# Optimization experiments

Hardware: AMD Instinct MI355X
Metric: run time of the kernel (lower is better)

The kernel has to match this reference:

```python
import jax, jax.numpy as jnp
import numpy as np

D_MODEL = 1024
NUM_EXP = 64
EPS = 1e-9
B, L = 16, 2048


def setup_inputs() -> dict:
    key = jax.random.key(0)
    ks = jax.random.split(key, 12)
    s = 1.0 / np.sqrt(D_MODEL)
    inp = {
        "x": jax.random.normal(ks[0], (B, L, D_MODEL), dtype=jnp.float32),
        "n_indexes": jax.random.randint(ks[1], (B, NUM_EXP), 0, NUM_EXP),
        "mask": jax.random.randint(ks[2], (B, 1, L), 0, 2).astype(jnp.int32),
        "q_emb": jax.random.normal(ks[3], (NUM_EXP, D_MODEL), dtype=jnp.float32),
        "b_emb": jax.random.normal(ks[4], (NUM_EXP, D_MODEL), dtype=jnp.float32),
        "Wk": jax.random.normal(ks[5], (D_MODEL, D_MODEL), dtype=jnp.float32) * s,
        "bk": jnp.zeros((D_MODEL,), jnp.float32),
        "Wa": jax.random.normal(ks[6], (D_MODEL, D_MODEL), dtype=jnp.float32) * s,
        "ba": jnp.zeros((D_MODEL,), jnp.float32),
        "Wb": jax.random.normal(ks[7], (D_MODEL, D_MODEL), dtype=jnp.float32) * s,
        "bb": jnp.zeros((D_MODEL,), jnp.float32),
        "Ws": jax.random.normal(ks[8], (D_MODEL, D_MODEL), dtype=jnp.float32) * s,
        "bs": jnp.zeros((D_MODEL,), jnp.float32),
    }
    return inp


def reference(x, n_indexes, mask, q_emb, b_emb, Wk, bk, Wa, ba, Wb, bb, Ws, bs):
    # Dropout layers act as identity (eval mode).
    query_exp = q_emb[n_indexes]          # [B, E, D]
    bias_exp = b_emb[n_indexes]           # [B, E, D]
    x_key = x @ Wk.T + bk                 # [B, L, D]
    z = jnp.einsum('bed,bld->bel', query_exp, x_key) / np.sqrt(D_MODEL)  # [B, E, L]

    maskf = (mask != 0).astype(z.dtype)   # broadcast [B,1,L]
    class_a_fw = jax.nn.relu(z) * maskf
    class_b_fw = jax.nn.relu(-z) * maskf
    class_a_fw = class_a_fw / (class_a_fw.sum(-1, keepdims=True) + EPS)
    class_b_fw = class_b_fw / (class_b_fw.sum(-1, keepdims=True) + EPS)

    class_a = jnp.einsum('bel,bld->bed', class_a_fw, x @ Wa.T + ba) + bias_exp
    class_b = jnp.einsum('bel,bld->bed', class_b_fw, x @ Wb.T + bb) + bias_exp

    zt = jnp.swapaxes(z, -2, -1)          # [B, L, E]  (unmasked, as in source)
    class_a_bw = jax.nn.relu(zt)
    class_b_bw = jax.nn.relu(-zt)
    class_a_bw = class_a_bw / (class_a_bw.sum(-1, keepdims=True) + EPS)
    class_b_bw = class_b_bw / (class_b_bw.sum(-1, keepdims=True) + EPS)

    class_a = jnp.einsum('ble,bed->bld', class_a_bw, class_a)  # [B, L, D]
    class_b = jnp.einsum('ble,bed->bld', class_b_bw, class_b)

    selector = jax.nn.sigmoid(x @ Ws.T + bs)
    return selector * class_a + (1.0 - selector) * class_b
```

## Files before the change

### kernel.cpp

```cpp
#include <hip/hip_runtime.h>
#include <math.h>

#define D_MODEL 1024
#define NUM_EXP 64
#define B_SZ 16
#define L_SZ 2048

using bf16x8  = __attribute__((ext_vector_type(8))) __bf16;
using floatx4 = __attribute__((ext_vector_type(4))) float;
using ushort8 = __attribute__((ext_vector_type(8))) unsigned short;
using ushort4v = __attribute__((ext_vector_type(4))) unsigned short;

__device__ __forceinline__ unsigned short f2bf(float f) {
    union { float f; unsigned u; } x; x.f = f;
    unsigned r = (x.u + 0x7fffu + ((x.u >> 16) & 1u)) >> 16;
    return (unsigned short)r;
}
__device__ __forceinline__ float bf2f(unsigned short h) {
    union { unsigned u; float f; } x; x.u = ((unsigned)h) << 16;
    return x.f;
}

#define GLD16(gp, lp) __builtin_amdgcn_global_load_lds( \
    (const __attribute__((address_space(1))) unsigned int*)(gp), \
    (__attribute__((address_space(3))) unsigned int*)(lp), 16, 0, 0)

__global__ void k_convx(const float* __restrict__ in, unsigned short* __restrict__ outN,
                        unsigned short* __restrict__ outT)
{
    __shared__ unsigned short T[64][65];
    const int b = blockIdx.z;
    const int l0 = blockIdx.y * 64, c0 = blockIdx.x * 64;
    const int t = threadIdx.x;
    const int tr = t >> 4, tc = (t & 15) * 4;
    const float* src = in + ((long)b * L_SZ + l0) * D_MODEL + c0;
    unsigned short* dN = outN + ((long)b * L_SZ + l0) * D_MODEL + c0;
    #pragma unroll
    for (int i = 0; i < 4; i++) {
        int r = tr + i * 16;
        float4 v = *(const float4*)(src + (long)r * D_MODEL + tc);
        ushort4v u; u[0]=f2bf(v.x); u[1]=f2bf(v.y); u[2]=f2bf(v.z); u[3]=f2bf(v.w);
        *(ushort4v*)(dN + (long)r * D_MODEL + tc) = u;
        T[r][tc+0]=u[0]; T[r][tc+1]=u[1]; T[r][tc+2]=u[2]; T[r][tc+3]=u[3];
    }
    __syncthreads();
    unsigned short* dT = outT + ((long)b * D_MODEL + c0) * L_SZ + l0;
    #pragma unroll
    for (int i = 0; i < 4; i++) {
        int c = tr + i * 16;
        ushort4v u;
        u[0]=T[tc+0][c]; u[1]=T[tc+1][c]; u[2]=T[tc+2][c]; u[3]=T[tc+3][c];
        *(ushort4v*)(dT + (long)c * L_SZ + tc) = u;
    }
}

__global__ void k_transw(const float* __restrict__ in, unsigned short* __restrict__ outT)
{
    __shared__ unsigned short T[64][65];
    const int r0 = blockIdx.y * 64, c0 = blockIdx.x * 64;
    const int t = threadIdx.x;
    const int tr = t >> 4, tc = (t & 15) * 4;
    const float* src = in + (long)r0 * D_MODEL + c0;
    #pragma unroll
    for (int i = 0; i < 4; i++) {
        int r = tr + i * 16;
        float4 v = *(const float4*)(src + (long)r * D_MODEL + tc);
        T[r][tc+0]=f2bf(v.x); T[r][tc+1]=f2bf(v.y); T[r][tc+2]=f2bf(v.z); T[r][tc+3]=f2bf(v.w);
    }
    __syncthreads();
    unsigned short* dT = outT + ((long)c0) * D_MODEL + r0;
    #pragma unroll
    for (int i = 0; i < 4; i++) {
        int c = tr + i * 16;
        ushort4v u;
        u[0]=T[tc+0][c]; u[1]=T[tc+1][c]; u[2]=T[tc+2][c]; u[3]=T[tc+3][c];
        *(ushort4v*)(dT + (long)c * D_MODEL + tc) = u;
    }
}

__global__ void k_convert3(const float* __restrict__ a, const float* __restrict__ b,
                           const float* __restrict__ c,
                           unsigned short* __restrict__ oa, unsigned short* __restrict__ ob,
                           unsigned short* __restrict__ oc)
{
    long i = ((long)blockIdx.x * 256 + threadIdx.x) * 8;
    int which = (int)(i >> 20);
    long off = i & ((1L << 20) - 1);
    const float* src = which == 0 ? a : which == 1 ? b : c;
    unsigned short* dst = which == 0 ? oa : which == 1 ? ob : oc;
    float4 v0 = *(const float4*)(src + off);
    float4 v1 = *(const float4*)(src + off + 4);
    ushort8 r;
    r[0]=f2bf(v0.x); r[1]=f2bf(v0.y); r[2]=f2bf(v0.z); r[3]=f2bf(v0.w);
    r[4]=f2bf(v1.x); r[5]=f2bf(v1.y); r[6]=f2bf(v1.z); r[7]=f2bf(v1.w);
    *(ushort8*)(dst + off) = r;
}

__global__ void k_gather(const int* __restrict__ idx, const float* __restrict__ q_emb,
                         const float* __restrict__ b_emb, const float* __restrict__ bk,
                         unsigned short* __restrict__ qexp, float* __restrict__ bias_exp,
                         float* __restrict__ qbk)
{
    int be = blockIdx.x;
    int row = idx[be];
    int t = threadIdx.x;
    const float* qs = q_emb + (long)row * D_MODEL;
    const float* bsrc = b_emb + (long)row * D_MODEL;
    float4 q4 = *(const float4*)(qs + t * 4);
    float4 k4 = *(const float4*)(bk + t * 4);
    float4 b4 = *(const float4*)(bsrc + t * 4);
    ushort4v r; r[0]=f2bf(q4.x); r[1]=f2bf(q4.y); r[2]=f2bf(q4.z); r[3]=f2bf(q4.w);
    *(ushort4v*)(qexp + (long)be * D_MODEL + t * 4) = r;
    *(float4*)(bias_exp + (long)be * D_MODEL + t * 4) = b4;
    float p = q4.x*k4.x + q4.y*k4.y + q4.z*k4.z + q4.w*k4.w;
    #pragma unroll
    for (int o = 32; o > 0; o >>= 1) p += __shfl_down(p, o);
    __shared__ float red[4];
    if ((t & 63) == 0) red[t >> 6] = p;
    __syncthreads();
    if (t == 0) qbk[be] = red[0] + red[1] + red[2] + red[3];
}

__launch_bounds__(256)
__global__ void k_gemm_bt(const unsigned short* __restrict__ A,
                          const unsigned short* __restrict__ Bm,
                          const float* __restrict__ rowbias,
                          void* __restrict__ Cout,
                          int M, int N, int K, float scale, int flags,
                          long sA, long sB, long sC)
{
    __shared__ __align__(16) unsigned short As[64 * 32];
    __shared__ __align__(16) unsigned short Bs[64 * 32];
    const int bz = blockIdx.z;
    const unsigned short* Ab = A + (long)bz * sA;
    const unsigned short* Bb = Bm + (long)bz * sB;
    const int tid = threadIdx.x;
    const int wave = tid >> 6, lane = tid & 63;
    const int m0 = blockIdx.y * 64, n0 = blockIdx.x * 64;
    const int lrow = tid >> 2, lk = (tid & 3) * 8;
    const int q = lane >> 4, mr = lane & 15;

    floatx4 acc[4];
    floatx4 z4 = {0.f, 0.f, 0.f, 0.f};
    #pragma unroll
    for (int j = 0; j < 4; j++) acc[j] = z4;

    const unsigned short* Aptr = Ab + (long)(m0 + lrow) * K + lk;
    const unsigned short* Bptr = Bb + (long)(n0 + lrow) * K + lk;

    for (int k0 = 0; k0 < K; k0 += 32) {
        __syncthreads();
        *(ushort8*)&As[lrow * 32 + lk] = *(const ushort8*)(Aptr + k0);
        *(ushort8*)&Bs[lrow * 32 + lk] = *(const ushort8*)(Bptr + k0);
        __syncthreads();
        bf16x8 af = *(const bf16x8*)&As[(wave * 16 + mr) * 32 + q * 8];
        #pragma unroll
        for (int j = 0; j < 4; j++) {
            bf16x8 bfr = *(const bf16x8*)&Bs[(j * 16 + mr) * 32 + q * 8];
            acc[j] = __builtin_amdgcn_mfma_f32_16x16x32_bf16(af, bfr, acc[j], 0, 0, 0);
        }
    }
    #pragma unroll
    for (int j = 0; j < 4; j++) {
        int gn = n0 + j * 16 + mr;
        #pragma unroll
        for (int r = 0; r < 4; r++) {
            int gm = m0 + wave * 16 + q * 4 + r;
            float v = acc[j][r];
            if (rowbias) v += rowbias[(long)bz * M + gm];
            v *= scale;
            long cidx = (long)bz * sC + (long)gm * N + gn;
            if (flags & 1) ((unsigned short*)Cout)[cidx] = f2bf(v);
            else           ((float*)Cout)[cidx] = v;
        }
    }
}

__launch_bounds__(256)
__global__ void k_gemm_fw2(const unsigned short* __restrict__ A1,
                           const unsigned short* __restrict__ A2,
                           const unsigned short* __restrict__ Bt,
                           unsigned short* __restrict__ C1,
                           unsigned short* __restrict__ C2)
{
    __shared__ __align__(16) unsigned short As1[64 * 32];
    __shared__ __align__(16) unsigned short As2[64 * 32];
    __shared__ __align__(16) unsigned short Bs[64 * 32];
    const int bz = blockIdx.z;
    const int n0 = blockIdx.x * 64;
    const int tid = threadIdx.x;
    const int wave = tid >> 6, lane = tid & 63;
    const int lrow = tid >> 2, lk = (tid & 3) * 8;
    const int q = lane >> 4, mr = lane & 15;

    const unsigned short* a1p = A1 + ((long)bz * NUM_EXP + lrow) * L_SZ + lk;
    const unsigned short* a2p = A2 + ((long)bz * NUM_EXP + lrow) * L_SZ + lk;
    const unsigned short* bp  = Bt + ((long)bz * D_MODEL + n0 + lrow) * L_SZ + lk;

    floatx4 acc1[4], acc2[4];
    floatx4 z4 = {0.f, 0.f, 0.f, 0.f};
    #pragma unroll
    for (int j = 0; j < 4; j++) { acc1[j] = z4; acc2[j] = z4; }

    for (int k0 = 0; k0 < L_SZ; k0 += 32) {
        __syncthreads();
        *(ushort8*)&As1[lrow * 32 + lk] = *(const ushort8*)(a1p + k0);
        *(ushort8*)&As2[lrow * 32 + lk] = *(const ushort8*)(a2p + k0);
        *(ushort8*)&Bs[lrow * 32 + lk]  = *(const ushort8*)(bp + k0);
        __syncthreads();
        bf16x8 f1 = *(const bf16x8*)&As1[(wave * 16 + mr) * 32 + q * 8];
        bf16x8 f2 = *(const bf16x8*)&As2[(wave * 16 + mr) * 32 + q * 8];
        #pragma unroll
        for (int j = 0; j < 4; j++) {
            bf16x8 bb = *(const bf16x8*)&Bs[(j * 16 + mr) * 32 + q * 8];
            acc1[j] = __builtin_amdgcn_mfma_f32_16x16x32_bf16(f1, bb, acc1[j], 0, 0, 0);
            acc2[j] = __builtin_amdgcn_mfma_f32_16x16x32_bf16(f2, bb, acc2[j], 0, 0, 0);
        }
    }
    #pragma unroll
    for (int j = 0; j < 4; j++) {
        int gn = n0 + j * 16 + mr;
        #pragma unroll
        for (int r = 0; r < 4; r++) {
            int gm = wave * 16 + q * 4 + r;
            long cidx = ((long)bz * NUM_EXP + gm) * D_MODEL + gn;
            C1[cidx] = f2bf(acc1[j][r]);
            C2[cidx] = f2bf(acc2[j][r]);
        }
    }
}

__launch_bounds__(256)
__global__ void k_gemm_cls(const unsigned short* __restrict__ fwxA, const unsigned short* __restrict__ fwxB,
                           const unsigned short* __restrict__ Wa_, const unsigned short* __restrict__ Wb_,
                           const float* __restrict__ ba_, const float* __restrict__ bb_,
                           const float* __restrict__ wsA, const float* __restrict__ wsB,
                           const float* __restrict__ biasE,
                           unsigned short* __restrict__ aHi, unsigned short* __restrict__ aLo,
                           unsigned short* __restrict__ bHi, unsigned short* __restrict__ bLo)
{
    __shared__ __align__(16) unsigned short As[64 * 32];
    __shared__ __align__(16) unsigned short Bs[64 * 32];
    const int zz = blockIdx.z;
    const int side = zz >> 4, bz = zz & 15;
    const unsigned short* Ab = (side ? fwxB : fwxA) + (long)bz * NUM_EXP * D_MODEL;
    const unsigned short* Bb = side ? Wb_ : Wa_;
    const float* cb = side ? bb_ : ba_;
    const float* rw = (side ? wsB : wsA) + bz * NUM_EXP;
    const float* bE = biasE + (long)bz * NUM_EXP * D_MODEL;
    unsigned short* oHi = (side ? bHi : aHi) + (long)bz * NUM_EXP * D_MODEL;
    unsigned short* oLo = (side ? bLo : aLo) + (long)bz * NUM_EXP * D_MODEL;

    const int tid = threadIdx.x;
    const int wave = tid >> 6, lane = tid & 63;
    const int n0 = blockIdx.x * 64;
    const int lrow = tid >> 2, lk = (tid & 3) * 8;
    const int q = lane >> 4, mr = lane & 15;

    floatx4 acc[4];
    floatx4 z4 = {0.f, 0.f, 0.f, 0.f};
    #pragma unroll
    for (int j = 0; j < 4; j++) acc[j] = z4;

    const unsigned short* Aptr = Ab + (long)lrow * D_MODEL + lk;
    const unsigned short* Bptr = Bb + (long)(n0 + lrow) * D_MODEL + lk;

    for (int k0 = 0; k0 < D_MODEL; k0 += 32) {
        __syncthreads();
        *(ushort8*)&As[lrow * 32 + lk] = *(const ushort8*)(Aptr + k0);
        *(ushort8*)&Bs[lrow * 32 + lk] = *(const ushort8*)(Bptr + k0);
        __syncthreads();
        bf16x8 af = *(const bf16x8*)&As[(wave * 16 + mr) * 32 + q * 8];
        #pragma unroll
        for (int j = 0; j < 4; j++) {
            bf16x8 bfr = *(const bf16x8*)&Bs[(j * 16 + mr) * 32 + q * 8];
            acc[j] = __builtin_amdgcn_mfma_f32_16x16x32_bf16(af, bfr, acc[j], 0, 0, 0);
        }
    }
    #pragma unroll
    for (int j = 0; j < 4; j++) {
        int gn = n0 + j * 16 + mr;
        float cbv = cb[gn];
        #pragma unroll
        for (int r = 0; r < 4; r++) {
            int gm = wave * 16 + q * 4 + r;
            float v = acc[j][r] + rw[gm] * cbv + bE[(long)gm * D_MODEL + gn];
            unsigned short hi = f2bf(v);
            long tix = (long)gn * NUM_EXP + gm;
            oHi[tix] = hi;
            oLo[tix] = f2bf(v - bf2f(hi));
        }
    }
}

__launch_bounds__(512, 2)
__global__ void k_gemm_sel(const unsigned short* __restrict__ A,
                           const unsigned short* __restrict__ Bm,
                           const float* __restrict__ bias,
                           unsigned short* __restrict__ C)
{
    __shared__ __align__(16) unsigned short As[2][2][8192];
    __shared__ __align__(16) unsigned short Bs[2][2][8192];

    const int tid = threadIdx.x;
    const int wid = tid >> 6, lane = tid & 63;
    const int q = lane >> 4, mr = lane & 15;
    const int wm = wid >> 2, wn = wid & 3;
    const int kread = (q ^ ((mr >> 1) & 3)) * 8;

    const int bid = blockIdx.x;
    const int wg = (bid & 7) * 64 + (bid >> 3);
    const int m0 = (wg >> 2) * 256;
    const int n0 = (wg & 3) * 256;

    const unsigned short* Ag = A + (long)m0 * 1024;
    const unsigned short* Bg = Bm + (long)n0 * 1024;

    const int srow = tid >> 2;
    const int sgrp = (tid & 3) ^ ((srow >> 1) & 3);
    const long soff = (long)srow * 1024 + sgrp * 8;
    const int ldst = wid * 64 * 8;

    auto STAGE = [&](int g) {
        int tile = g >> 2; if (tile > 15) tile = 15;
        const int kh = (g >> 1) & 1, isB = g & 1;
        const unsigned short* src = (isB ? Bg : Ag) + (long)tile * 64 + kh * 32 + soff;
        unsigned short* dst = (isB ? &Bs[0][0][0] : &As[0][0][0])
                              + ((tile & 1) * 2 + kh) * 8192 + ldst;
        GLD16(src, dst);
        GLD16(src + 128 * 1024, dst + 4096);
    };

    floatx4 acc[8][4];
    floatx4 z4 = {0.f, 0.f, 0.f, 0.f};
    #pragma unroll
    for (int i = 0; i < 8; i++)
        #pragma unroll
        for (int j = 0; j < 4; j++) acc[i][j] = z4;

    STAGE(0); STAGE(1); STAGE(2); STAGE(3); STAGE(4); STAGE(5);
    asm volatile("s_waitcnt vmcnt(4)" ::: "memory");
    __builtin_amdgcn_s_barrier();

    for (int t = 0; t < 16; t++) {
        const unsigned short* Abuf = &As[t & 1][0][0];
        const unsigned short* Bbuf = &Bs[t & 1][0][0];
        bf16x8 bfr[4];
        #pragma unroll
        for (int p = 0; p < 4; p++) {
            const int kh = p >> 1, mh = p & 1;
            bf16x8 af[4];
            #pragma unroll
            for (int i = 0; i < 4; i++)
                af[i] = *(const bf16x8*)&Abuf[kh * 8192 +
                        (wm * 128 + mh * 64 + i * 16 + mr) * 32 + kread];
            if (mh == 0) {
                #pragma unroll
                for (int j = 0; j < 4; j++)
                    bfr[j] = *(const bf16x8*)&Bbuf[kh * 8192 +
                             (wn * 64 + j * 16 + mr) * 32 + kread];
            }
            STAGE(4 * t + p + 6);
            if (mh == 1) asm volatile("s_waitcnt vmcnt(8)" ::: "memory");
            __builtin_amdgcn_s_barrier();
            asm volatile("s_waitcnt lgkmcnt(0)" ::: "memory");
            __builtin_amdgcn_sched_barrier(0);
            __builtin_amdgcn_s_setprio(1);
            #pragma unroll
            for (int i = 0; i < 4; i++)
                #pragma unroll
                for (int j = 0; j < 4; j++)
                    acc[mh * 4 + i][j] = __builtin_amdgcn_mfma_f32_16x16x32_bf16(
                        af[i], bfr[j], acc[mh * 4 + i][j], 0, 0, 0);
            __builtin_amdgcn_s_setprio(0);
            __builtin_amdgcn_s_barrier();
            __builtin_amdgcn_sched_barrier(0);
        }
    }
    asm volatile("s_waitcnt vmcnt(0)" ::: "memory");

    #pragma unroll
    for (int i = 0; i < 8; i++) {
        #pragma unroll
        for (int j = 0; j < 4; j++) {
            const int gn = n0 + wn * 64 + j * 16 + mr;
            const float cbv = bias[gn];
            #pragma unroll
            for (int r = 0; r < 4; r++) {
                const int gm = m0 + wm * 128 + i * 16 + q * 4 + r;
                C[(long)gm * 1024 + gn] = f2bf(acc[i][j][r] + cbv);
            }
        }
    }
}

__global__ void k_fwnorm(const float* __restrict__ z, const int* __restrict__ mask,
                         unsigned short* __restrict__ a_fw, unsigned short* __restrict__ b_fw,
                         float* __restrict__ wsum_a, float* __restrict__ wsum_b)
{
    int be = blockIdx.x;
    int b = be >> 6;
    const float* zr = z + (long)be * L_SZ;
    const int* mr = mask + (long)b * L_SZ;
    int tid = threadIdx.x;
    float sa = 0.f, sb = 0.f;
    for (int l = tid; l < L_SZ; l += 256) {
        float v = zr[l];
        if (mr[l] != 0) { sa += fmaxf(v, 0.f); sb += fmaxf(-v, 0.f); }
    }
    #pragma unroll
    for (int o = 32; o > 0; o >>= 1) { sa += __shfl_down(sa, o); sb += __shfl_down(sb, o); }
    __shared__ float red[8];
    int wave = tid >> 6, lane = tid & 63;
    if (lane == 0) { red[wave] = sa; red[4 + wave] = sb; }
    __syncthreads();
    float ta = red[0] + red[1] + red[2] + red[3];
    float tb = red[4] + red[5] + red[6] + red[7];
    float ia = 1.f / (ta + 1e-9f), ib = 1.f / (tb + 1e-9f);
    if (tid == 0) { wsum_a[be] = ta * ia; wsum_b[be] = tb * ib; }
    for (int l = tid; l < L_SZ; l += 256) {
        float v = zr[l];
        float m = (mr[l] != 0) ? 1.f : 0.f;
        a_fw[(long)be * L_SZ + l] = f2bf(fmaxf(v, 0.f) * m * ia);
        b_fw[(long)be * L_SZ + l] = f2bf(fmaxf(-v, 0.f) * m * ib);
    }
}

__global__ void k_bwnorm(const float* __restrict__ z, unsigned short* __restrict__ a_bw,
                         unsigned short* __restrict__ b_bw)
{
    int r = blockIdx.x * 256 + threadIdx.x;
    int b = r >> 11, l = r & 2047;
    const float* zb = z + (long)b * NUM_EXP * L_SZ + l;
    float sa = 0.f, sb = 0.f;
    float va[NUM_EXP];
    #pragma unroll 8
    for (int e = 0; e < NUM_EXP; e++) {
        float v = zb[(long)e * L_SZ];
        va[e] = v;
        sa += fmaxf(v, 0.f); sb += fmaxf(-v, 0.f);
    }
    float ia = 1.f / (sa + 1e-9f), ib = 1.f / (sb + 1e-9f);
    unsigned short* ar = a_bw + (long)r * NUM_EXP;
    unsigned short* br = b_bw + (long)r * NUM_EXP;
    #pragma unroll 8
    for (int e = 0; e < NUM_EXP; e++) {
        float v = va[e];
        ar[e] = f2bf(fmaxf(v, 0.f) * ia);
        br[e] = f2bf(fmaxf(-v, 0.f) * ib);
    }
}

__launch_bounds__(256)
__global__ void k_final_mfma(const unsigned short* __restrict__ aw,
                             const unsigned short* __restrict__ bw,
                             const unsigned short* __restrict__ caHi,
                             const unsigned short* __restrict__ caLo,
                             const unsigned short* __restrict__ cbHi,
                             const unsigned short* __restrict__ cbLo,
                             const unsigned short* __restrict__ selbf,
                             float* __restrict__ out)
{
    __shared__ __align__(16) unsigned short Aa[64 * 72];
    __shared__ __align__(16) unsigned short Ab[64 * 72];
    __shared__ __align__(16) unsigned short BaH[64 * 72];
    __shared__ __align__(16) unsigned short BaL[64 * 72];
    __shared__ __align__(16) unsigned short BbH[64 * 72];
    __shared__ __align__(16) unsigned short BbL[64 * 72];
    const int bz = blockIdx.z;
    const int l0 = blockIdx.y * 64, d0 = blockIdx.x * 64;
    const int tid = threadIdx.x;
    const int wave = tid >> 6, lane = tid & 63;
    const int q = lane >> 4, mr = lane & 15;

    const unsigned short* awb = aw + ((long)bz * L_SZ + l0) * NUM_EXP;
    const unsigned short* bwb = bw + ((long)bz * L_SZ + l0) * NUM_EXP;
    const long cbase = ((long)bz * D_MODEL + d0) * NUM_EXP;

    #pragma unroll
    for (int c = 0; c < 2; c++) {
        int idx = c * 256 + tid;
        int row = idx >> 3, kc = (idx & 7) * 8;
        int lw = row * 72 + kc;
        long ga = (long)row * NUM_EXP + kc;
        *(ushort8*)&Aa[lw]  = *(const ushort8*)(awb + ga);
        *(ushort8*)&Ab[lw]  = *(const ushort8*)(bwb + ga);
        *(ushort8*)&BaH[lw] = *(const ushort8*)(caHi + cbase + ga);
        *(ushort8*)&BaL[lw] = *(const ushort8*)(caLo + cbase + ga);
        *(ushort8*)&BbH[lw] = *(const ushort8*)(cbHi + cbase + ga);
        *(ushort8*)&BbL[lw] = *(const ushort8*)(cbLo + cbase + ga);
    }
    __syncthreads();

    floatx4 accA[4], accB[4];
    floatx4 z4 = {0.f, 0.f, 0.f, 0.f};
    #pragma unroll
    for (int j = 0; j < 4; j++) { accA[j] = z4; accB[j] = z4; }

    #pragma unroll
    for (int ks = 0; ks < 2; ks++) {
        int ko = ks * 32 + q * 8;
        bf16x8 fa = *(const bf16x8*)&Aa[(wave * 16 + mr) * 72 + ko];
        bf16x8 fb = *(const bf16x8*)&Ab[(wave * 16 + mr) * 72 + ko];
        #pragma unroll
        for (int j = 0; j < 4; j++) {
            int bo = (j * 16 + mr) * 72 + ko;
            accA[j] = __builtin_amdgcn_mfma_f32_16x16x32_bf16(fa, *(const bf16x8*)&BaH[bo], accA[j], 0, 0, 0);
            accA[j] = __builtin_amdgcn_mfma_f32_16x16x32_bf16(fa, *(const bf16x8*)&BaL[bo], accA[j], 0, 0, 0);
            accB[j] = __builtin_amdgcn_mfma_f32_16x16x32_bf16(fb, *(const bf16x8*)&BbH[bo], accB[j], 0, 0, 0);
            accB[j] = __builtin_amdgcn_mfma_f32_16x16x32_bf16(fb, *(const bf16x8*)&BbL[bo], accB[j], 0, 0, 0);
        }
    }

    #pragma unroll
    for (int j = 0; j < 4; j++) {
        #pragma unroll
        for (int r = 0; r < 4; r++) {
            int gl = l0 + wave * 16 + q * 4 + r;
            int gd = d0 + j * 16 + mr;
            long o = ((long)bz * L_SZ + gl) * D_MODEL + gd;
            float s = 1.f / (1.f + __expf(-bf2f(selbf[o])));
            out[o] = s * accA[j][r] + (1.f - s) * accB[j][r];
        }
    }
}

extern "C" void kernel_launch(void* const* d_in, const int* in_sizes, int n_in,
                              void* d_out, int out_size, void* d_ws, size_t ws_size,
                              hipStream_t stream)
{
    const float* x     = (const float*)d_in[0];
    const int*   nidx  = (const int*)d_in[1];
    const int*   mask  = (const int*)d_in[2];
    const float* q_emb = (const float*)d_in[3];
    const float* b_emb = (const float*)d_in[4];
    const float* Wk    = (const float*)d_in[5];
    const float* bk    = (const float*)d_in[6];
    const float* Wa    = (const float*)d_in[7];
    const float* ba    = (const float*)d_in[8];
    const float* Wb    = (const float*)d_in[9];
    const float* bb    = (const float*)d_in[10];
    const float* Ws    = (const float*)d_in[11];
    const float* bs    = (const float*)d_in[12];
    float* out = (float*)d_out;

    constexpr long BLD = (long)B_SZ * L_SZ * D_MODEL;
    constexpr long BEL = (long)B_SZ * NUM_EXP * L_SZ;
    constexpr long BED = (long)B_SZ * NUM_EXP * D_MODEL;
    constexpr long DD  = (long)D_MODEL * D_MODEL;

    char* w = (char*)d_ws;
    size_t off = 0;
    auto carve = [&](size_t bytes) { char* p = w + off; off += (bytes + 255) & ~(size_t)255; return p; };
    unsigned short* x_bf   = (unsigned short*)carve(BLD * 2);
    unsigned short* x_bfT  = (unsigned short*)carve(BLD * 2);
    unsigned short* wkT_bf = (unsigned short*)carve(DD * 2);
    unsigned short* wa_bf  = (unsigned short*)carve(DD * 2);
    unsigned short* wb_bf  = (unsigned short*)carve(DD * 2);
    unsigned short* ws_bf  = (unsigned short*)carve(DD * 2);
    unsigned short* qexp   = (unsigned short*)carve(BED * 2);
    float*          bias_e = (float*)carve(BED * 4);
    float*          qbk    = (float*)carve(B_SZ * NUM_EXP * 4);
    unsigned short* qk     = (unsigned short*)carve(BED * 2);
    float*          z      = (float*)carve(BEL * 4);
    unsigned short* a_fw   = (unsigned short*)carve(BEL * 2);
    unsigned short* b_fw   = (unsigned short*)carve(BEL * 2);
    float*          wsum_a = (float*)carve(B_SZ * NUM_EXP * 4);
    float*          wsum_b = (float*)carve(B_SZ * NUM_EXP * 4);
    unsigned short* a_bw   = (unsigned short*)carve(BEL * 2);
    unsigned short* b_bw   = (unsigned short*)carve(BEL * 2);
    unsigned short* fwx_a  = (unsigned short*)carve(BED * 2);
    unsigned short* fwx_b  = (unsigned short*)carve(BED * 2);
    unsigned short* caHi   = (unsigned short*)carve(BED * 2);
    unsigned short* caLo   = (unsigned short*)carve(BED * 2);
    unsigned short* cbHi   = (unsigned short*)carve(BED * 2);
    unsigned short* cbLo   = (unsigned short*)carve(BED * 2);
    if (ws_size < off) return;
    unsigned short* selbf = x_bfT;

    k_convx<<<dim3(16, 32, B_SZ), 256, 0, stream>>>(x, x_bf, x_bfT);
    k_transw<<<dim3(16, 16), 256, 0, stream>>>(Wk, wkT_bf);
    k_convert3<<<(3 * DD) / 2048, 256, 0, stream>>>(Wa, Wb, Ws, wa_bf, wb_bf, ws_bf);
    k_gather<<<B_SZ * NUM_EXP, 256, 0, stream>>>(nidx, q_emb, b_emb, bk, qexp, bias_e, qbk);

    k_gemm_bt<<<dim3(16, 1, B_SZ), 256, 0, stream>>>(qexp, wkT_bf, nullptr, qk,
        NUM_EXP, D_MODEL, D_MODEL, 1.f, 1, (long)NUM_EXP * D_MODEL, 0, (long)NUM_EXP * D_MODEL);

    k_gemm_bt<<<dim3(32, 1, B_SZ), 256, 0, stream>>>(qk, x_bf, qbk, z,
        NUM_EXP, L_SZ, D_MODEL, 1.f / 32.f, 0,
        (long)NUM_EXP * D_MODEL, (long)L_SZ * D_MODEL, (long)NUM_EXP * L_SZ);

    k_fwnorm<<<B_SZ * NUM_EXP, 256, 0, stream>>>(z, mask, a_fw, b_fw, wsum_a, wsum_b);
    k_bwnorm<<<(B_SZ * L_SZ) / 256, 256, 0, stream>>>(z, a_bw, b_bw);

    k_gemm_fw2<<<dim3(16, 1, B_SZ), 256, 0, stream>>>(a_fw, b_fw, x_bfT, fwx_a, fwx_b);

    k_gemm_sel<<<512, 512, 0, stream>>>(x_bf, ws_bf, bs, selbf);

    k_gemm_cls<<<dim3(16, 1, 32), 256, 0, stream>>>(fwx_a, fwx_b, wa_bf, wb_bf, ba, bb,
        wsum_a, wsum_b, bias_e, caHi, caLo, cbHi, cbLo);

    k_final_mfma<<<dim3(16, 32, B_SZ), 256, 0, stream>>>(a_bw, b_bw, caHi, caLo, cbHi, cbLo, selbf, out);
}
```

Measured before the change: 548.4 us.

## Merge prep and norm kernels, split-K fw2 GEMM, halve sel GEMM grid

Combines the Wk transpose, the weight conversion and the gather into one k_prep launch, and combines the forward and backward normalisations into one k_norms launch, which removes launch overhead. k_gemm_fw2 becomes a 512-thread block that splits the L reduction between two groups and adds the partials through shared memory. With only 256 blocks, this targets the low occupancy of that GEMM. k_gemm_sel now has each workgroup compute two adjacent 256-wide N tiles in sequence, halving its grid, at the cost of fewer parallel blocks and a longer serial loop.

```diff
diff --git a/kernel.cpp b/kernel.cpp
--- a/kernel.cpp
+++ b/kernel.cpp
@@ -54,71 +54,70 @@
     }
 }
 
-__global__ void k_transw(const float* __restrict__ in, unsigned short* __restrict__ outT)
+__global__ void k_prep(const float* __restrict__ Wk,
+                       const float* __restrict__ Wa, const float* __restrict__ Wb,
+                       const float* __restrict__ Ws,
+                       const int* __restrict__ idx, const float* __restrict__ q_emb,
+                       const float* __restrict__ b_emb, const float* __restrict__ bk,
+                       unsigned short* __restrict__ wkT,
+                       unsigned short* __restrict__ oa, unsigned short* __restrict__ ob,
+                       unsigned short* __restrict__ oc,
+                       unsigned short* __restrict__ qexp, float* __restrict__ bias_exp,
+                       float* __restrict__ qbk)
 {
     __shared__ unsigned short T[64][65];
-    const int r0 = blockIdx.y * 64, c0 = blockIdx.x * 64;
+    __shared__ float red[4];
+    const int blk = blockIdx.x;
     const int t = threadIdx.x;
-    const int tr = t >> 4, tc = (t & 15) * 4;
-    const float* src = in + (long)r0 * D_MODEL + c0;
-    #pragma unroll
-    for (int i = 0; i < 4; i++) {
-        int r = tr + i * 16;
-        float4 v = *(const float4*)(src + (long)r * D_MODEL + tc);
-        T[r][tc+0]=f2bf(v.x); T[r][tc+1]=f2bf(v.y); T[r][tc+2]=f2bf(v.z); T[r][tc+3]=f2bf(v.w);
-    }
-    __syncthreads();
-    unsigned short* dT = outT + ((long)c0) * D_MODEL + r0;
-    #pragma unroll
-    for (int i = 0; i < 4; i++) {
-        int c = tr + i * 16;
-        ushort4v u;
-        u[0]=T[tc+0][c]; u[1]=T[tc+1][c]; u[2]=T[tc+2][c]; u[3]=T[tc+3][c];
-        *(ushort4v*)(dT + (long)c * D_MODEL + tc) = u;
-    }
-}
-
-__global__ void k_convert3(const float* __restrict__ a, const float* __restrict__ b,
-                           const float* __restrict__ c,
-                           unsigned short* __restrict__ oa, unsigned short* __restrict__ ob,
-                           unsigned short* __restrict__ oc)
-{
-    long i = ((long)blockIdx.x * 256 + threadIdx.x) * 8;
-    int which = (int)(i >> 20);
-    long off = i & ((1L << 20) - 1);
-    const float* src = which == 0 ? a : which == 1 ? b : c;
-    unsigned short* dst = which == 0 ? oa : which == 1 ? ob : oc;
-    float4 v0 = *(const float4*)(src + off);
-    float4 v1 = *(const float4*)(src + off + 4);
-    ushort8 r;
-    r[0]=f2bf(v0.x); r[1]=f2bf(v0.y); r[2]=f2bf(v0.z); r[3]=f2bf(v0.w);
-    r[4]=f2bf(v1.x); r[5]=f2bf(v1.y); r[6]=f2bf(v1.z); r[7]=f2bf(v1.w);
-    *(ushort8*)(dst + off) = r;
-}
-
-__global__ void k_gather(const int* __restrict__ idx, const float* __restrict__ q_emb,
-                         const float* __restrict__ b_emb, const float* __restrict__ bk,
-                         unsigned short* __restrict__ qexp, float* __restrict__ bias_exp,
-                         float* __restrict__ qbk)
-{
-    int be = blockIdx.x;
-    int row = idx[be];
-    int t = threadIdx.x;
-    const float* qs = q_emb + (long)row * D_MODEL;
-    const float* bsrc = b_emb + (long)row * D_MODEL;
-    float4 q4 = *(const float4*)(qs + t * 4);
-    float4 k4 = *(const float4*)(bk + t * 4);
-    float4 b4 = *(const float4*)(bsrc + t * 4);
-    ushort4v r; r[0]=f2bf(q4.x); r[1]=f2bf(q4.y); r[2]=f2bf(q4.z); r[3]=f2bf(q4.w);
-    *(ushort4v*)(qexp + (long)be * D_MODEL + t * 4) = r;
-    *(float4*)(bias_exp + (long)be * D_MODEL + t * 4) = b4;
-    float p = q4.x*k4.x + q4.y*k4.y + q4.z*k4.z + q4.w*k4.w;
-    #pragma unroll
-    for (int o = 32; o > 0; o >>= 1) p += __shfl_down(p, o);
-    __shared__ float red[4];
-    if ((t & 63) == 0) red[t >> 6] = p;
-    __syncthreads();
-    if (t == 0) qbk[be] = red[0] + red[1] + red[2] + red[3];
+    if (blk < 256) {
+        const int r0 = (blk >> 4) * 64, c0 = (blk & 15) * 64;
+        const int tr = t >> 4, tc = (t & 15) * 4;
+        const float* src = Wk + (long)r0 * D_MODEL + c0;
+        #pragma unroll
+        for (int i = 0; i < 4; i++) {
+            int r = tr + i * 16;
+            float4 v = *(const float4*)(src + (long)r * D_MODEL + tc);
+            T[r][tc+0]=f2bf(v.x); T[r][tc+1]=f2bf(v.y); T[r][tc+2]=f2bf(v.z); T[r][tc+3]=f2bf(v.w);
+        }
+        __syncthreads();
+        unsigned short* dT = wkT + ((long)c0) * D_MODEL + r0;
+        #pragma unroll
+        for (int i = 0; i < 4; i++) {
+            int c = tr + i * 16;
+            ushort4v u;
+            u[0]=T[tc+0][c]; u[1]=T[tc+1][c]; u[2]=T[tc+2][c]; u[3]=T[tc+3][c];
+            *(ushort4v*)(dT + (long)c * D_MODEL + tc) = u;
+        }
+    } else if (blk < 256 + 1536) {
+        long i = ((long)(blk - 256) * 256 + t) * 8;
+        int which = (int)(i >> 20);
+        long off = i & ((1L << 20) - 1);
+        const float* src = which == 0 ? Wa : which == 1 ? Wb : Ws;
+        unsigned short* dst = which == 0 ? oa : which == 1 ? ob : oc;
+        float4 v0 = *(const float4*)(src + off);
+        float4 v1 = *(const float4*)(src + off + 4);
+        ushort8 r;
+        r[0]=f2bf(v0.x); r[1]=f2bf(v0.y); r[2]=f2bf(v0.z); r[3]=f2bf(v0.w);
+        r[4]=f2bf(v1.x); r[5]=f2bf(v1.y); r[6]=f2bf(v1.z); r[7]=f2bf(v1.w);
+        *(ushort8*)(dst + off) = r;
+    } else {
+        const int be = blk - 1792;
+        const int row = idx[be];
+        const float* qs = q_emb + (long)row * D_MODEL;
+        const float* bsrc = b_emb + (long)row * D_MODEL;
+        float4 q4 = *(const float4*)(qs + t * 4);
+        float4 k4 = *(const float4*)(bk + t * 4);
+        float4 b4 = *(const float4*)(bsrc + t * 4);
+        ushort4v r; r[0]=f2bf(q4.x); r[1]=f2bf(q4.y); r[2]=f2bf(q4.z); r[3]=f2bf(q4.w);
+        *(ushort4v*)(qexp + (long)be * D_MODEL + t * 4) = r;
+        *(float4*)(bias_exp + (long)be * D_MODEL + t * 4) = b4;
+        float p = q4.x*k4.x + q4.y*k4.y + q4.z*k4.z + q4.w*k4.w;
+        #pragma unroll
+        for (int o = 32; o > 0; o >>= 1) p += __shfl_down(p, o);
+        if ((t & 63) == 0) red[t >> 6] = p;
+        __syncthreads();
+        if (t == 0) qbk[be] = red[0] + red[1] + red[2] + red[3];
+    }
 }
 
 __launch_bounds__(256)
@@ -176,56 +175,74 @@
     }
 }
 
-__launch_bounds__(256)
+__launch_bounds__(512)
 __global__ void k_gemm_fw2(const unsigned short* __restrict__ A1,
                            const unsigned short* __restrict__ A2,
                            const unsigned short* __restrict__ Bt,
                            unsigned short* __restrict__ C1,
                            unsigned short* __restrict__ C2)
 {
-    __shared__ __align__(16) unsigned short As1[64 * 32];
-    __shared__ __align__(16) unsigned short As2[64 * 32];
-    __shared__ __align__(16) unsigned short Bs[64 * 32];
+    __shared__ __align__(16) unsigned short As1[2][64 * 32];
+    __shared__ __align__(16) unsigned short As2[2][64 * 32];
+    __shared__ __align__(16) unsigned short Bs[2][64 * 32];
+    __shared__ float Red[2][64][65];
     const int bz = blockIdx.z;
     const int n0 = blockIdx.x * 64;
     const int tid = threadIdx.x;
-    const int wave = tid >> 6, lane = tid & 63;
-    const int lrow = tid >> 2, lk = (tid & 3) * 8;
+    const int grp = tid >> 8;
+    const int gtid = tid & 255;
+    const int wave = gtid >> 6, lane = tid & 63;
+    const int lrow = gtid >> 2, lk = (gtid & 3) * 8;
     const int q = lane >> 4, mr = lane & 15;
-
-    const unsigned short* a1p = A1 + ((long)bz * NUM_EXP + lrow) * L_SZ + lk;
-    const unsigned short* a2p = A2 + ((long)bz * NUM_EXP + lrow) * L_SZ + lk;
-    const unsigned short* bp  = Bt + ((long)bz * D_MODEL + n0 + lrow) * L_SZ + lk;
+    const int kb = grp * (L_SZ / 2);
+
+    const unsigned short* a1p = A1 + ((long)bz * NUM_EXP + lrow) * L_SZ + kb + lk;
+    const unsigned short* a2p = A2 + ((long)bz * NUM_EXP + lrow) * L_SZ + kb + lk;
+    const unsigned short* bp  = Bt + ((long)bz * D_MODEL + n0 + lrow) * L_SZ + kb + lk;
 
     floatx4 acc1[4], acc2[4];
     floatx4 z4 = {0.f, 0.f, 0.f, 0.f};
     #pragma unroll
     for (int j = 0; j < 4; j++) { acc1[j] = z4; acc2[j] = z4; }
 
-    for (int k0 = 0; k0 < L_SZ; k0 += 32) {
-        __syncthreads();
-        *(ushort8*)&As1[lrow * 32 + lk] = *(const ushort8*)(a1p + k0);
-        *(ushort8*)&As2[lrow * 32 + lk] = *(const ushort8*)(a2p + k0);
-        *(ushort8*)&Bs[lrow * 32 + lk]  = *(const ushort8*)(bp + k0);
-        __syncthreads();
-        bf16x8 f1 = *(const bf16x8*)&As1[(wave * 16 + mr) * 32 + q * 8];
-        bf16x8 f2 = *(const bf16x8*)&As2[(wave * 16 + mr) * 32 + q * 8];
+    for (int k0 = 0; k0 < L_SZ / 2; k0 += 32) {
+        __syncthreads();
+        *(ushort8*)&As1[grp][lrow * 32 + lk] = *(const ushort8*)(a1p + k0);
+        *(ushort8*)&As2[grp][lrow * 32 + lk] = *(const ushort8*)(a2p + k0);
+        *(ushort8*)&Bs[grp][lrow * 32 + lk]  = *(const ushort8*)(bp + k0);
+        __syncthreads();
+        bf16x8 f1 = *(const bf16x8*)&As1[grp][(wave * 16 + mr) * 32 + q * 8];
+        bf16x8 f2 = *(const bf16x8*)&As2[grp][(wave * 16 + mr) * 32 + q * 8];
         #pragma unroll
         for (int j = 0; j < 4; j++) {
-            bf16x8 bb = *(const bf16x8*)&Bs[(j * 16 + mr) * 32 + q * 8];
+            bf16x8 bb = *(const bf16x8*)&Bs[grp][(j * 16 + mr) * 32 + q * 8];
             acc1[j] = __builtin_amdgcn_mfma_f32_16x16x32_bf16(f1, bb, acc1[j], 0, 0, 0);
             acc2[j] = __builtin_amdgcn_mfma_f32_16x16x32_bf16(f2, bb, acc2[j], 0, 0, 0);
         }
     }
-    #pragma unroll
-    for (int j = 0; j < 4; j++) {
-        int gn = n0 + j * 16 + mr;
-        #pragma unroll
-        for (int r = 0; r < 4; r++) {
-            int gm = wave * 16 + q * 4 + r;
-            long cidx = ((long)bz * NUM_EXP + gm) * D_MODEL + gn;
-            C1[cidx] = f2bf(acc1[j][r]);
-            C2[cidx] = f2bf(acc2[j][r]);
+    __syncthreads();
+    if (grp == 1) {
+        #pragma unroll
+        for (int j = 0; j < 4; j++)
+            #pragma unroll
+            for (int r = 0; r < 4; r++) {
+                int gm = wave * 16 + q * 4 + r;
+                Red[0][gm][j * 16 + mr] = acc1[j][r];
+                Red[1][gm][j * 16 + mr] = acc2[j][r];
+            }
+    }
+    __syncthreads();
+    if (grp == 0) {
+        #pragma unroll
+        for (int j = 0; j < 4; j++) {
+            int gn = n0 + j * 16 + mr;
+            #pragma unroll
+            for (int r = 0; r < 4; r++) {
+                int gm = wave * 16 + q * 4 + r;
+                long cidx = ((long)bz * NUM_EXP + gm) * D_MODEL + gn;
+                C1[cidx] = f2bf(acc1[j][r] + Red[0][gm][j * 16 + mr]);
+                C2[cidx] = f2bf(acc2[j][r] + Red[1][gm][j * 16 + mr]);
+            }
         }
     }
 }
@@ -309,12 +326,13 @@
     const int kread = (q ^ ((mr >> 1) & 3)) * 8;
 
     const int bid = blockIdx.x;
-    const int wg = (bid & 7) * 64 + (bid >> 3);
-    const int m0 = (wg >> 2) * 256;
-    const int n0 = (wg & 3) * 256;
+    const int wg = (bid & 7) * 32 + (bid >> 3);
+    const int m0 = (wg >> 1) * 256;
+    const int npair = wg & 1;
 
     const unsigned short* Ag = A + (long)m0 * 1024;
-    const unsigned short* Bg = Bm + (long)n0 * 1024;
+    const unsigned short* Bg0 = Bm + (long)(npair * 512) * 1024;
+    const unsigned short* Bg1 = Bg0 + (long)256 * 1024;
 
     const int srow = tid >> 2;
     const int sgrp = (tid & 3) ^ ((srow >> 1) & 3);
@@ -322,11 +340,13 @@
     const int ldst = wid * 64 * 8;
 
     auto STAGE = [&](int g) {
-        int tile = g >> 2; if (tile > 15) tile = 15;
+        int T = g >> 2; if (T > 31) T = 31;
         const int kh = (g >> 1) & 1, isB = g & 1;
-        const unsigned short* src = (isB ? Bg : Ag) + (long)tile * 64 + kh * 32 + soff;
+        const int tl = T & 15;
+        const unsigned short* base = isB ? (T < 16 ? Bg0 : Bg1) : Ag;
+        const unsigned short* src = base + (long)tl * 64 + kh * 32 + soff;
         unsigned short* dst = (isB ? &Bs[0][0][0] : &As[0][0][0])
-                              + ((tile & 1) * 2 + kh) * 8192 + ldst;
+                              + ((tl & 1) * 2 + kh) * 8192 + ldst;
         GLD16(src, dst);
         GLD16(src + 128 * 1024, dst + 4096);
     };
@@ -342,112 +362,115 @@
     asm volatile("s_waitcnt vmcnt(4)" ::: "memory");
     __builtin_amdgcn_s_barrier();
 
-    for (int t = 0; t < 16; t++) {
-        const unsigned short* Abuf = &As[t & 1][0][0];
-        const unsigned short* Bbuf = &Bs[t & 1][0][0];
-        bf16x8 bfr[4];
-        #pragma unroll
-        for (int p = 0; p < 4; p++) {
-            const int kh = p >> 1, mh = p & 1;
-            bf16x8 af[4];
+    for (int h = 0; h < 2; h++) {
+        for (int t = 0; t < 16; t++) {
+            const unsigned short* Abuf = &As[t & 1][0][0];
+            const unsigned short* Bbuf = &Bs[t & 1][0][0];
+            bf16x8 bfr[4];
             #pragma unroll
-            for (int i = 0; i < 4; i++)
-                af[i] = *(const bf16x8*)&Abuf[kh * 8192 +
-                        (wm * 128 + mh * 64 + i * 16 + mr) * 32 + kread];
-            if (mh == 0) {
+            for (int p = 0; p < 4; p++) {
+                const int kh = p >> 1, mh = p & 1;
+                bf16x8 af[4];
                 #pragma unroll
-                for (int j = 0; j < 4; j++)
-                    bfr[j] = *(const bf16x8*)&Bbuf[kh * 8192 +
-                             (wn * 64 + j * 16 + mr) * 32 + kread];
+                for (int i = 0; i < 4; i++)
+                    af[i] = *(const bf16x8*)&Abuf[kh * 8192 +
+                            (wm * 128 + mh * 64 + i * 16 + mr) * 32 + kread];
+                if (mh == 0) {
+                    #pragma unroll
+                    for (int j = 0; j < 4; j++)
+                        bfr[j] = *(const bf16x8*)&Bbuf[kh * 8192 +
+                                 (wn * 64 + j * 16 + mr) * 32 + kread];
+                }
+                STAGE(h * 64 + 4 * t + p + 6);
+                if (mh == 1) asm volatile("s_waitcnt vmcnt(8)" ::: "memory");
+                __builtin_amdgcn_s_barrier();
+                asm volatile("s_waitcnt lgkmcnt(0)" ::: "memory");
+                __builtin_amdgcn_sched_barrier(0);
+                __builtin_amdgcn_s_setprio(1);
+                #pragma unroll
+                for (int i = 0; i < 4; i++)
+                    #pragma unroll
+                    for (int j = 0; j < 4; j++)
+                        acc[mh * 4 + i][j] = __builtin_amdgcn_mfma_f32_16x16x32_bf16(
+                            af[i], bfr[j], acc[mh * 4 + i][j], 0, 0, 0);
+                __builtin_amdgcn_s_setprio(0);
+                __builtin_amdgcn_s_barrier();
+                __builtin_amdgcn_sched_barrier(0);
             }
-            STAGE(4 * t + p + 6);
-            if (mh == 1) asm volatile("s_waitcnt vmcnt(8)" ::: "memory");
-            __builtin_amdgcn_s_barrier();
-            asm volatile("s_waitcnt lgkmcnt(0)" ::: "memory");
-            __builtin_amdgcn_sched_barrier(0);
-            __builtin_amdgcn_s_setprio(1);
+        }
+        const int n0 = npair * 512 + h * 256;
+        #pragma unroll
+        for (int i = 0; i < 8; i++) {
             #pragma unroll
-            for (int i = 0; i < 4; i++)
+            for (int j = 0; j < 4; j++) {
+                const int gn = n0 + wn * 64 + j * 16 + mr;
+                const float cbv = bias[gn];
                 #pragma unroll
-                for (int j = 0; j < 4; j++)
-                    acc[mh * 4 + i][j] = __builtin_amdgcn_mfma_f32_16x16x32_bf16(
-                        af[i], bfr[j], acc[mh * 4 + i][j], 0, 0, 0);
-            __builtin_amdgcn_s_setprio(0);
-            __builtin_amdgcn_s_barrier();
-            __builtin_amdgcn_sched_barrier(0);
+                for (int r = 0; r < 4; r++) {
+                    const int gm = m0 + wm * 128 + i * 16 + q * 4 + r;
+                    C[(long)gm * 1024 + gn] = f2bf(acc[i][j][r] + cbv);
+                    if (h == 0) acc[i][j][r] = 0.f;
+                }
+            }
         }
     }
     asm volatile("s_waitcnt vmcnt(0)" ::: "memory");
-
-    #pragma unroll
-    for (int i = 0; i < 8; i++) {
-        #pragma unroll
-        for (int j = 0; j < 4; j++) {
-            const int gn = n0 + wn * 64 + j * 16 + mr;
-            const float cbv = bias[gn];
-            #pragma unroll
-            for (int r = 0; r < 4; r++) {
-                const int gm = m0 + wm * 128 + i * 16 + q * 4 + r;
-                C[(long)gm * 1024 + gn] = f2bf(acc[i][j][r] + cbv);
-            }
-        }
-    }
-}
-
-__global__ void k_fwnorm(const float* __restrict__ z, const int* __restrict__ mask,
-                         unsigned short* __restrict__ a_fw, unsigned short* __restrict__ b_fw,
-                         float* __restrict__ wsum_a, float* __restrict__ wsum_b)
-{
-    int be = blockIdx.x;
-    int b = be >> 6;
-    const float* zr = z + (long)be * L_SZ;
-    const int* mr = mask + (long)b * L_SZ;
-    int tid = threadIdx.x;
-    float sa = 0.f, sb = 0.f;
-    for (int l = tid; l < L_SZ; l += 256) {
-        float v = zr[l];
-        if (mr[l] != 0) { sa += fmaxf(v, 0.f); sb += fmaxf(-v, 0.f); }
-    }
-    #pragma unroll
-    for (int o = 32; o > 0; o >>= 1) { sa += __shfl_down(sa, o); sb += __shfl_down(sb, o); }
-    __shared__ float red[8];
-    int wave = tid >> 6, lane = tid & 63;
-    if (lane == 0) { red[wave] = sa; red[4 + wave] = sb; }
-    __syncthreads();
-    float ta = red[0] + red[1] + red[2] + red[3];
-    float tb = red[4] + red[5] + red[6] + red[7];
-    float ia = 1.f / (ta + 1e-9f), ib = 1.f / (tb + 1e-9f);
-    if (tid == 0) { wsum_a[be] = ta * ia; wsum_b[be] = tb * ib; }
-    for (int l = tid; l < L_SZ; l += 256) {
-        float v = zr[l];
-        float m = (mr[l] != 0) ? 1.f : 0.f;
-        a_fw[(long)be * L_SZ + l] = f2bf(fmaxf(v, 0.f) * m * ia);
-        b_fw[(long)be * L_SZ + l] = f2bf(fmaxf(-v, 0.f) * m * ib);
-    }
-}
-
-__global__ void k_bwnorm(const float* __restrict__ z, unsigned short* __restrict__ a_bw,
-                         unsigned short* __restrict__ b_bw)
-{
-    int r = blockIdx.x * 256 + threadIdx.x;
-    int b = r >> 11, l = r & 2047;
-    const float* zb = z + (long)b * NUM_EXP * L_SZ + l;
-    float sa = 0.f, sb = 0.f;
-    float va[NUM_EXP];
-    #pragma unroll 8
-    for (int e = 0; e < NUM_EXP; e++) {
-        float v = zb[(long)e * L_SZ];
-        va[e] = v;
-        sa += fmaxf(v, 0.f); sb += fmaxf(-v, 0.f);
-    }
-    float ia = 1.f / (sa + 1e-9f), ib = 1.f / (sb + 1e-9f);
-    unsigned short* ar = a_bw + (long)r * NUM_EXP;
-    unsigned short* br = b_bw + (long)r * NUM_EXP;
-    #pragma unroll 8
-    for (int e = 0; e < NUM_EXP; e++) {
-        float v = va[e];
-        ar[e] = f2bf(fmaxf(v, 0.f) * ia);
-        br[e] = f2bf(fmaxf(-v, 0.f) * ib);
+}
+
+__global__ void k_norms(const float* __restrict__ z, const int* __restrict__ mask,
+                        unsigned short* __restrict__ a_fw, unsigned short* __restrict__ b_fw,
+                        float* __restrict__ wsum_a, float* __restrict__ wsum_b,
+                        unsigned short* __restrict__ a_bw, unsigned short* __restrict__ b_bw)
+{
+    const int blk = blockIdx.x;
+    const int tid = threadIdx.x;
+    if (blk < 1024) {
+        const int be = blk;
+        const int b = be >> 6;
+        const float* zr = z + (long)be * L_SZ;
+        const int* mr = mask + (long)b * L_SZ;
+        float sa = 0.f, sb = 0.f;
+        for (int l = tid; l < L_SZ; l += 256) {
+            float v = zr[l];
+            if (mr[l] != 0) { sa += fmaxf(v, 0.f); sb += fmaxf(-v, 0.f); }
+        }
+        #pragma unroll
+        for (int o = 32; o > 0; o >>= 1) { sa += __shfl_down(sa, o); sb += __shfl_down(sb, o); }
+        __shared__ float red[8];
+        int wave = tid >> 6, lane = tid & 63;
+        if (lane == 0) { red[wave] = sa; red[4 + wave] = sb; }
+        __syncthreads();
+        float ta = red[0] + red[1] + red[2] + red[3];
+        float tb = red[4] + red[5] + red[6] + red[7];
+        float ia = 1.f / (ta + 1e-9f), ib = 1.f / (tb + 1e-9f);
+        if (tid == 0) { wsum_a[be] = ta * ia; wsum_b[be] = tb * ib; }
+        for (int l = tid; l < L_SZ; l += 256) {
+            float v = zr[l];
+            float m = (mr[l] != 0) ? 1.f : 0.f;
+            a_fw[(long)be * L_SZ + l] = f2bf(fmaxf(v, 0.f) * m * ia);
+            b_fw[(long)be * L_SZ + l] = f2bf(fmaxf(-v, 0.f) * m * ib);
+        }
+    } else {
+        int r = (blk - 1024) * 256 + tid;
+        int b = r >> 11, l = r & 2047;
+        const float* zb = z + (long)b * NUM_EXP * L_SZ + l;
+        float sa = 0.f, sb = 0.f;
+        float va[NUM_EXP];
+        #pragma unroll 8
+        for (int e = 0; e < NUM_EXP; e++) {
+            float v = zb[(long)e * L_SZ];
+            va[e] = v;
+            sa += fmaxf(v, 0.f); sb += fmaxf(-v, 0.f);
+        }
+        float ia = 1.f / (sa + 1e-9f), ib = 1.f / (sb + 1e-9f);
+        unsigned short* ar = a_bw + (long)r * NUM_EXP;
+        unsigned short* br = b_bw + (long)r * NUM_EXP;
+        #pragma unroll 8
+        for (int e = 0; e < NUM_EXP; e++) {
+            float v = va[e];
+            ar[e] = f2bf(fmaxf(v, 0.f) * ia);
+            br[e] = f2bf(fmaxf(-v, 0.f) * ib);
+        }
     }
 }
 
@@ -579,9 +602,8 @@
     unsigned short* selbf = x_bfT;
 
     k_convx<<<dim3(16, 32, B_SZ), 256, 0, stream>>>(x, x_bf, x_bfT);
-    k_transw<<<dim3(16, 16), 256, 0, stream>>>(Wk, wkT_bf);
-    k_convert3<<<(3 * DD) / 2048, 256, 0, stream>>>(Wa, Wb, Ws, wa_bf, wb_bf, ws_bf);
-    k_gather<<<B_SZ * NUM_EXP, 256, 0, stream>>>(nidx, q_emb, b_emb, bk, qexp, bias_e, qbk);
+    k_prep<<<2816, 256, 0, stream>>>(Wk, Wa, Wb, Ws, nidx, q_emb, b_emb, bk,
+                                     wkT_bf, wa_bf, wb_bf, ws_bf, qexp, bias_e, qbk);
 
     k_gemm_bt<<<dim3(16, 1, B_SZ), 256, 0, stream>>>(qexp, wkT_bf, nullptr, qk,
         NUM_EXP, D_MODEL, D_MODEL, 1.f, 1, (long)NUM_EXP * D_MODEL, 0, (long)NUM_EXP * D_MODEL);
@@ -590,12 +612,11 @@
         NUM_EXP, L_SZ, D_MODEL, 1.f / 32.f, 0,
         (long)NUM_EXP * D_MODEL, (long)L_SZ * D_MODEL, (long)NUM_EXP * L_SZ);
 
-    k_fwnorm<<<B_SZ * NUM_EXP, 256, 0, stream>>>(z, mask, a_fw, b_fw, wsum_a, wsum_b);
-    k_bwnorm<<<(B_SZ * L_SZ) / 256, 256, 0, stream>>>(z, a_bw, b_bw);
-
-    k_gemm_fw2<<<dim3(16, 1, B_SZ), 256, 0, stream>>>(a_fw, b_fw, x_bfT, fwx_a, fwx_b);
-
-    k_gemm_sel<<<512, 512, 0, stream>>>(x_bf, ws_bf, bs, selbf);
+    k_norms<<<1152, 256, 0, stream>>>(z, mask, a_fw, b_fw, wsum_a, wsum_b, a_bw, b_bw);
+
+    k_gemm_fw2<<<dim3(16, 1, B_SZ), 512, 0, stream>>>(a_fw, b_fw, x_bfT, fwx_a, fwx_b);
+
+    k_gemm_sel<<<256, 512, 0, stream>>>(x_bf, ws_bf, bs, selbf);
 
     k_gemm_cls<<<dim3(16, 1, 32), 256, 0, stream>>>(fwx_a, fwx_b, wa_bf, wb_bf, ba, bb,
         wsum_a, wsum_b, bias_e, caHi, caLo, cbHi, cbLo);
```

Result: faster. 523.6 us (-4.5%).
